# Performance work log

Hardware: AMD Instinct MI355X
Metric: run time of the kernel (lower is better)

## Reference

```python
import jax, jax.numpy as jnp
import numpy as np

T = 32400   # bs*H*W BEV queries (1*180*180)
S = 16896   # bs*num_cams*h*w image keys (1*6*32*88)
E = 256     # embed_dim
H = 8       # num_heads
D = 32      # head_dim
MAXL = 32   # max interval length (ref_num_f)


def _mlp(x, w1, b1, w2, b2):
    # nn.Sequential(Linear(E,2E), ReLU, Linear(2E,E))
    return jax.nn.relu(x @ w1 + b1) @ w2 + b2


def setup_inputs() -> dict:
    k0 = jax.random.key(0)
    ks = jax.random.split(k0, 8)
    # ragged interval structure: every BEV cell has an interval of length (idx%32)+1
    lengths = (np.arange(T) % MAXL) + 1
    starts = np.concatenate([np.zeros(1, np.int64), np.cumsum(lengths)[:-1]])
    N = int(lengths.sum())  # 534472 frustum points
    ranks_bev = np.repeat(np.arange(T), lengths)          # sorted by BEV cell
    rng = np.random.default_rng(0)
    ranks_feat = rng.integers(0, S, size=N)               # which key/value row each point reads

    def lin(k, fi, fo):
        return jax.random.normal(k, (fi, fo), jnp.float32) * (1.0 / np.sqrt(fi))

    key_feat = jax.random.normal(ks[1], (S, E), jnp.float32)
    return dict(
        query_depth=jax.random.normal(ks[0], (T, E), jnp.float32),
        key=key_feat,
        value=key_feat,  # module asserts torch.equal(key, value)
        q_w1=lin(ks[2], E, 2 * E), q_b1=jnp.zeros((2 * E,), jnp.float32),
        q_w2=lin(ks[3], 2 * E, E), q_b2=jnp.zeros((E,), jnp.float32),
        k_w1=lin(ks[4], E, 2 * E), k_b1=jnp.zeros((2 * E,), jnp.float32),
        k_w2=lin(ks[5], 2 * E, E), k_b2=jnp.zeros((E,), jnp.float32),
        ranks_feat_f=jnp.asarray(ranks_feat, jnp.int32),
        ranks_bev_f=jnp.asarray(ranks_bev, jnp.int32),
        interval_starts_f=jnp.asarray(starts, jnp.int32),
        interval_lengths_f=jnp.asarray(lengths, jnp.int32),
        ref_num=MAXL,
    )


def reference(query_depth, key, value,
              q_w1, q_b1, q_w2, q_b2,
              k_w1, k_b1, k_w2, k_b2,
              ranks_feat_f, ranks_bev_f,
              interval_starts_f, interval_lengths_f, ref_num):
    scaling = 1.0 / jnp.sqrt(jnp.float32(D))
    q = (_mlp(query_depth, q_w1, q_b1, q_w2, q_b2) * scaling).reshape(T, H, D)
    k = _mlp(key, k_w1, k_b1, k_w2, k_b2).reshape(S, H, D)
    v = value.reshape(S, H, D)

    N = ranks_bev_f.shape[0]
    pt = jnp.arange(N, dtype=jnp.int32)
    # interval id of each point (intervals are contiguous, sorted by start)
    iid = jnp.searchsorted(interval_starts_f, pt, side='right') - 1
    ranks_ref = pt - interval_starts_f[iid]  # within-interval slot, in [0, ref_num)

    # per-point raw attention logit: q[bev] . k[feat] per head  -> [N, H]
    w = jnp.einsum('nhd,nhd->nh', q[ranks_bev_f], k[ranks_feat_f])

    # scatter into ragged weight tensor [T, H, ref_num]; padding masked to -1e9
    attn = jnp.full((T, H, ref_num), -1e9, jnp.float32)
    attn = attn.at[ranks_bev_f, :, ranks_ref].set(w)
    attn = jax.nn.softmax(attn, axis=-1)

    # gather normalized weights back per point and scatter-combine values
    wp = attn[ranks_bev_f, :, ranks_ref]          # [N, H]
    vp = v[ranks_feat_f]                          # [N, H, D]
    out = jnp.zeros((T, H, D), jnp.float32).at[ranks_bev_f].add(wp[:, :, None] * vp)
    return out.reshape(T, E)
```

## Files before the change

kernel.cpp:

```cpp
#include <hip/hip_runtime.h>
#include <hip/hip_bf16.h>
#include <cstdint>
#include <cstddef>

constexpr int T_Q   = 32400;
constexpr int T_PAD = 32512;
constexpr int S_K   = 16896;
constexpr int E_DIM = 256;
constexpr int HID   = 512;

typedef __bf16 bf16x8 __attribute__((ext_vector_type(8)));
typedef float  f32x4  __attribute__((ext_vector_type(4)));
typedef unsigned short ushort8v __attribute__((ext_vector_type(8)));

__device__ __forceinline__ void async16(const __hip_bfloat16* gp, __hip_bfloat16* lp) {
    __builtin_amdgcn_global_load_lds(
        (const __attribute__((address_space(1))) void*)(gp),
        (__attribute__((address_space(3))) void*)(lp), 16, 0, 0);
}

__device__ __forceinline__ float b2f(unsigned short u) {
    return __uint_as_float(((unsigned)u) << 16);
}

constexpr int NB_K = (S_K * E_DIM / 4) / 256;
constexpr int NB_PREP = NB_K + 128;

__global__ __launch_bounds__(256) void prep(
    const float* __restrict__ val_in,
    const float* __restrict__ s0, const float* __restrict__ s1,
    const float* __restrict__ s2, const float* __restrict__ s3,
    __hip_bfloat16* __restrict__ kvB,
    __hip_bfloat16* __restrict__ d0, __hip_bfloat16* __restrict__ d1,
    __hip_bfloat16* __restrict__ d2, __hip_bfloat16* __restrict__ d3) {
    __shared__ float tb[64][65];
    const int b = blockIdx.x;
    const int tid = threadIdx.x;

    if (b < NB_K) {
        int i = (b * 256 + tid) * 4;
        float4 f = *(const float4*)(val_in + i);
        union { ushort4 u4; __hip_bfloat16 bb[4]; } cv;
        cv.bb[0] = __float2bfloat16(f.x);
        cv.bb[1] = __float2bfloat16(f.y);
        cv.bb[2] = __float2bfloat16(f.z);
        cv.bb[3] = __float2bfloat16(f.w);
        int r = i >> 8, c = i & 255;
        *(ushort4*)(kvB + (size_t)r * 512 + 256 + c) = cv.u4;
        return;
    }

    int tloc = b - NB_K;
    int m = tloc >> 5;
    int tt = tloc & 31;
    const float* S = m == 0 ? s0 : m == 1 ? s1 : m == 2 ? s2 : s3;
    __hip_bfloat16* D = m == 0 ? d0 : m == 1 ? d1 : m == 2 ? d2 : d3;
    int Kd, Nd, kt, nt;
    if ((m & 1) == 0) { Kd = 256; Nd = 512; kt = tt & 3; nt = tt >> 2; }
    else              { Kd = 512; Nd = 256; kt = tt & 7; nt = tt >> 3; }
    int tx = tid & 63, ty = tid >> 6;
#pragma unroll
    for (int p = 0; p < 16; ++p) {
        int row = ty * 16 + p;
        tb[row][tx] = S[(size_t)(kt * 64 + row) * Nd + nt * 64 + tx];
    }
    __syncthreads();
#pragma unroll
    for (int p = 0; p < 16; ++p) {
        int row = ty * 16 + p;
        D[(size_t)(nt * 64 + row) * Kd + kt * 64 + tx] = __float2bfloat16(tb[tx][row]);
    }
}


constexpr int MLP_QT = T_PAD / 64;
constexpr int MLP_KT = S_K / 64;
constexpr int MLP_NB = MLP_QT + MLP_KT;

__global__ __launch_bounds__(512, 4) void mlp_fused(
    const float* __restrict__ Aq, const float* __restrict__ Ak,
    const __hip_bfloat16* __restrict__ W1q, const __hip_bfloat16* __restrict__ W1k,
    const __hip_bfloat16* __restrict__ W2q, const __hip_bfloat16* __restrict__ W2k,
    const float* __restrict__ b1q, const float* __restrict__ b1k,
    const float* __restrict__ b2q, const float* __restrict__ b2k,
    __hip_bfloat16* __restrict__ Cq, __hip_bfloat16* __restrict__ Ck,
    float scaleq, int qtiles) {
    __shared__ __align__(16) __hip_bfloat16 Aslab[64 * 64];
    __shared__ __align__(16) __hip_bfloat16 Bs[256 * 64];
    __shared__ __align__(16) __hip_bfloat16 Hs[64 * 256];

    const int b = blockIdx.x;
    const bool isq = b < qtiles;
    const float* A  = isq ? Aq : Ak;
    const __hip_bfloat16* W1 = isq ? W1q : W1k;
    const __hip_bfloat16* W2 = isq ? W2q : W2k;
    const float* b1 = isq ? b1q : b1k;
    const float* b2 = isq ? b2q : b2k;
    __hip_bfloat16* C = isq ? Cq : Ck;
    const int ldc = isq ? E_DIM : 512;
    const float scale = isq ? scaleq : 1.0f;
    const int mrow0 = (isq ? b : b - qtiles) * 64;
    const int rowlim = isq ? T_Q : S_K;

    const int tid = threadIdx.x;
    const int w = tid >> 6, l = tid & 63;
    const int lm = l & 15, lq = l >> 4;
    const int wm = w >> 2;
    const int wn4 = w & 3;
    const int srow8 = l >> 3;
    const int u8 = l & 7;
    const int pu8 = u8 ^ srow8;
    const int scolB = (u8 ^ srow8) << 3;

    f32x4 acc2[2][4] = {};

#pragma unroll 1
    for (int nh = 0; nh < 2; ++nh) {
        f32x4 acc[2][4] = {};
#pragma unroll 1
        for (int st = 0; st < 4; ++st) {
            const int k0 = st * 64;
            {
                int r = w * 8 + srow8;
                int gr = mrow0 + r;
                float4 f0 = make_float4(0.f, 0.f, 0.f, 0.f);
                float4 f1 = make_float4(0.f, 0.f, 0.f, 0.f);
                if (gr < rowlim) {
                    const float* ap = A + (size_t)gr * 256 + k0 + u8 * 8;
                    f0 = *(const float4*)ap;
                    f1 = *(const float4*)(ap + 4);
                }
                union { bf16x8 v; __hip_bfloat16 bb[8]; } cv;
                cv.bb[0] = __float2bfloat16(f0.x); cv.bb[1] = __float2bfloat16(f0.y);
                cv.bb[2] = __float2bfloat16(f0.z); cv.bb[3] = __float2bfloat16(f0.w);
                cv.bb[4] = __float2bfloat16(f1.x); cv.bb[5] = __float2bfloat16(f1.y);
                cv.bb[6] = __float2bfloat16(f1.z); cv.bb[7] = __float2bfloat16(f1.w);
                *(bf16x8*)(Aslab + r * 64 + pu8 * 8) = cv.v;
            }
#pragma unroll
            for (int c = 0; c < 4; ++c) {
                int r = w * 32 + c * 8 + srow8;
                async16(W1 + (size_t)(nh * 256 + r) * 256 + k0 + scolB,
                        Bs + (w * 32 + c * 8) * 64);
            }
            __syncthreads();
#pragma unroll
            for (int ks = 0; ks < 2; ++ks) {
                bf16x8 af[2], bfr[4];
#pragma unroll
                for (int mi = 0; mi < 2; ++mi) {
                    int row = wm * 32 + mi * 16 + lm;
                    int pu = (ks * 4 + lq) ^ (row & 7);
                    af[mi] = *(const bf16x8*)(Aslab + row * 64 + pu * 8);
                }
#pragma unroll
                for (int ni = 0; ni < 4; ++ni) {
                    int brow = wn4 * 64 + ni * 16 + lm;
                    int pu = (ks * 4 + lq) ^ (brow & 7);
                    bfr[ni] = *(const bf16x8*)(Bs + brow * 64 + pu * 8);
                }
#pragma unroll
                for (int mi = 0; mi < 2; ++mi)
#pragma unroll
                    for (int ni = 0; ni < 4; ++ni)
                        acc[mi][ni] = __builtin_amdgcn_mfma_f32_16x16x32_bf16(
                            af[mi], bfr[ni], acc[mi][ni], 0, 0, 0);
            }
            __syncthreads();
        }

#pragma unroll
        for (int ni = 0; ni < 4; ++ni) {
            int col = wn4 * 64 + ni * 16 + lm;
            float bv = b1[nh * 256 + col];
            int un = col >> 3, el = col & 7;
#pragma unroll
            for (int mi = 0; mi < 2; ++mi) {
#pragma unroll
                for (int r = 0; r < 4; ++r) {
                    int row = wm * 32 + mi * 16 + lq * 4 + r;
                    float vv = fmaxf(acc[mi][ni][r] + bv, 0.f);
                    int pu = (un & 24) | ((un & 7) ^ (row & 7));
                    Hs[row * 256 + pu * 8 + el] = __float2bfloat16(vv);
                }
            }
        }

#pragma unroll 1
        for (int st = 0; st < 4; ++st) {
            const int k0 = st * 64;
#pragma unroll
            for (int c = 0; c < 4; ++c) {
                int r = w * 32 + c * 8 + srow8;
                async16(W2 + (size_t)r * 512 + nh * 256 + k0 + scolB,
                        Bs + (w * 32 + c * 8) * 64);
            }
            __syncthreads();
#pragma unroll
            for (int ks = 0; ks < 2; ++ks) {
                bf16x8 af[2], bfr[4];
#pragma unroll
                for (int mi = 0; mi < 2; ++mi) {
                    int row = wm * 32 + mi * 16 + lm;
                    int un = st * 8 + ks * 4 + lq;
                    int pu = (un & 24) | ((un & 7) ^ (row & 7));
                    af[mi] = *(const bf16x8*)(Hs + row * 256 + pu * 8);
                }
#pragma unroll
                for (int ni = 0; ni < 4; ++ni) {
                    int brow = wn4 * 64 + ni * 16 + lm;
                    int pu = (ks * 4 + lq) ^ (brow & 7);
                    bfr[ni] = *(const bf16x8*)(Bs + brow * 64 + pu * 8);
                }
#pragma unroll
                for (int mi = 0; mi < 2; ++mi)
#pragma unroll
                    for (int ni = 0; ni < 4; ++ni)
                        acc2[mi][ni] = __builtin_amdgcn_mfma_f32_16x16x32_bf16(
                            af[mi], bfr[ni], acc2[mi][ni], 0, 0, 0);
            }
            __syncthreads();
        }
    }

#pragma unroll
    for (int ni = 0; ni < 4; ++ni) {
        int col = wn4 * 64 + ni * 16 + lm;
        float bv = b2[col];
#pragma unroll
        for (int mi = 0; mi < 2; ++mi) {
            size_t rowb = (size_t)mrow0 + wm * 32 + mi * 16 + lq * 4;
#pragma unroll
            for (int r = 0; r < 4; ++r) {
                float vv = (acc2[mi][ni][r] + bv) * scale;
                C[(rowb + r) * ldc + col] = __float2bfloat16(vv);
            }
        }
    }
}


#define PREFP(KB, VB, C)                                                     \
    {                                                                        \
        int f_ = __shfl(myf, (C) + half);                                    \
        const __hip_bfloat16* p_ = kv + ((size_t)f_ << 9) + (sub << 3);      \
        KB = *(const ushort8v*)p_;                                           \
        VB = *(const ushort8v*)(p_ + 256);                                   \
    }

#define PROCP(KB, VB, C)                                                     \
    {                                                                        \
        float wv = 0.f;                                                      \
        _Pragma("unroll") for (int i = 0; i < 8; ++i)                        \
            wv = fmaf(qf[i], b2f(KB[i]), wv);                                \
        wv += __shfl_xor(wv, 1);                                             \
        wv += __shfl_xor(wv, 2);                                             \
        float sc = ((C) + half < L) ? wv : -1e30f;                           \
        float so = __shfl_xor(sc, 32);                                       \
        float pm = fmaxf(sc, so);                                            \
        if (__all(pm <= m)) {                                                \
            float p = __expf(sc - m);                                        \
            s += p;                                                          \
            _Pragma("unroll") for (int i = 0; i < 8; ++i)                    \
                a[i] = fmaf(p, b2f(VB[i]), a[i]);                            \
        } else {                                                             \
            float mn = fmaxf(m, pm);                                         \
            float al = __expf(m - mn);                                       \
            float p  = __expf(sc - mn);                                      \
            m = mn;                                                          \
            s = fmaf(s, al, p);                                              \
            _Pragma("unroll") for (int i = 0; i < 8; ++i)                    \
                a[i] = fmaf(p, b2f(VB[i]), a[i] * al);                       \
        }                                                                    \
    }

#define STEPP(KB, VB, J)                                                     \
    if (c + (J) < L) {                                                       \
        PROCP(KB, VB, c + (J));                                              \
        if (c + (J) + 8 < L) PREFP(KB, VB, c + (J) + 8);                     \
    }

constexpr int ATTN_BLOCKS = 2026;

__global__ __launch_bounds__(256) void attn_kernel(
    const __hip_bfloat16* __restrict__ q,
    const __hip_bfloat16* __restrict__ kv,
    const int* __restrict__ rf,
    const int* __restrict__ starts,
    const int* __restrict__ lens,
    float* __restrict__ out) {
    const int wid = threadIdx.x >> 6;
    const int l = threadIdx.x & 63;
    const int sub = l & 31, half = l >> 5;
    const int tstride = gridDim.x * 4;

    for (int t = blockIdx.x * 4 + wid; t < T_Q; t += tstride) {
        int su = __builtin_amdgcn_readfirstlane(starts[t]);
        int L  = __builtin_amdgcn_readfirstlane(lens[t]);

        int li = l < L - 1 ? l : L - 1;
        int myf = rf[su + li];

        ushort8v qu = *(const ushort8v*)(q + (size_t)t * 256 + sub * 8);
        float qf[8];
#pragma unroll
        for (int i = 0; i < 8; ++i) qf[i] = b2f(qu[i]);

        float m = -INFINITY, s = 0.f;
        float a[8] = {0.f, 0.f, 0.f, 0.f, 0.f, 0.f, 0.f, 0.f};

        ushort8v k0 = {}, v0 = {}, k1 = {}, v1 = {};
        ushort8v k2 = {}, v2 = {}, k3 = {}, v3 = {};
        PREFP(k0, v0, 0);
        if (L > 2) PREFP(k1, v1, 2);
        if (L > 4) PREFP(k2, v2, 4);
        if (L > 6) PREFP(k3, v3, 6);

        for (int c = 0; c < L; c += 8) {
            STEPP(k0, v0, 0)
            STEPP(k1, v1, 2)
            STEPP(k2, v2, 4)
            STEPP(k3, v3, 6)
        }

        float st = s + __shfl_xor(s, 32);
#pragma unroll
        for (int i = 0; i < 8; ++i) a[i] += __shfl_xor(a[i], 32);

        if (half) {
            float inv = 1.f / st;
            float* op = out + (size_t)t * 256 + sub * 8;
            float4 o0, o1;
            o0.x = a[0] * inv; o0.y = a[1] * inv; o0.z = a[2] * inv; o0.w = a[3] * inv;
            o1.x = a[4] * inv; o1.y = a[5] * inv; o1.z = a[6] * inv; o1.w = a[7] * inv;
            *(float4*)op = o0;
            *(float4*)(op + 4) = o1;
        }
    }
}

extern "C" void kernel_launch(void* const* d_in, const int* in_sizes, int n_in,
                              void* d_out, int out_size, void* d_ws, size_t ws_size,
                              hipStream_t stream) {
    const float* q_in   = (const float*)d_in[0];
    const float* key_in = (const float*)d_in[1];
    const float* val_in = (const float*)d_in[2];
    const float* q_w1   = (const float*)d_in[3];
    const float* q_b1   = (const float*)d_in[4];
    const float* q_w2   = (const float*)d_in[5];
    const float* q_b2   = (const float*)d_in[6];
    const float* k_w1   = (const float*)d_in[7];
    const float* k_b1   = (const float*)d_in[8];
    const float* k_w2   = (const float*)d_in[9];
    const float* k_b2   = (const float*)d_in[10];
    const int* ranks_feat = (const int*)d_in[11];
    const int* starts     = (const int*)d_in[13];
    const int* lens       = (const int*)d_in[14];
    float* out = (float*)d_out;

    char* ws = (char*)d_ws;
    size_t off = 0;
    auto alloc = [&](size_t bytes) {
        char* p = ws + off;
        off += (bytes + 255) & ~(size_t)255;
        return p;
    };
    __hip_bfloat16* qMl  = (__hip_bfloat16*)alloc((size_t)T_PAD * E_DIM * 2);
    __hip_bfloat16* kvB  = (__hip_bfloat16*)alloc((size_t)S_K * 512 * 2);
    __hip_bfloat16* w1qT = (__hip_bfloat16*)alloc((size_t)HID * E_DIM * 2);
    __hip_bfloat16* w2qT = (__hip_bfloat16*)alloc((size_t)E_DIM * HID * 2);
    __hip_bfloat16* w1kT = (__hip_bfloat16*)alloc((size_t)HID * E_DIM * 2);
    __hip_bfloat16* w2kT = (__hip_bfloat16*)alloc((size_t)E_DIM * HID * 2);
    (void)ws_size; (void)n_in; (void)out_size; (void)in_sizes;

    prep<<<NB_PREP, 256, 0, stream>>>(val_in, q_w1, q_w2, k_w1, k_w2,
                                      kvB, w1qT, w2qT, w1kT, w2kT);

    const float qscale = 0.17677669529663687f;

    mlp_fused<<<MLP_NB, 512, 0, stream>>>(
        q_in, key_in, w1qT, w1kT, w2qT, w2kT,
        q_b1, k_b1, q_b2, k_b2, qMl, kvB, qscale, MLP_QT);

    attn_kernel<<<ATTN_BLOCKS, 256, 0, stream>>>(qMl, kvB, ranks_feat, starts, lens, out);
}
```

Before: 273.4 us.

## Double-buffer MLP weight tiles and preload full input slab into LDS

The fused MLP kernel now stages the whole 64x256 input row slab into LDS once, converted to bf16, instead of reloading a 64-column slice at each K step. Weight tiles for W1 and W2 are ping-ponged between two LDS buffers, so the next tile's async global-to-LDS load is issued before the MFMA work on the current tile. The aim is to hide weight-load latency behind compute and remove one barrier per step. In exchange, LDS use grows to about 128KB per block and the launch-bounds occupancy hint is dropped, which likely allows fewer resident blocks per CU.

New measurement: 270.6 us. No clear change (-1.1%).

```diff
diff --git a/kernel.cpp b/kernel.cpp
--- a/kernel.cpp
+++ b/kernel.cpp
@@ -77,7 +77,7 @@
 constexpr int MLP_KT = S_K / 64;
 constexpr int MLP_NB = MLP_QT + MLP_KT;
 
-__global__ __launch_bounds__(512, 4) void mlp_fused(
+__global__ __launch_bounds__(512) void mlp_fused(
     const float* __restrict__ Aq, const float* __restrict__ Ak,
     const __hip_bfloat16* __restrict__ W1q, const __hip_bfloat16* __restrict__ W1k,
     const __hip_bfloat16* __restrict__ W2q, const __hip_bfloat16* __restrict__ W2k,
@@ -85,9 +85,9 @@
     const float* __restrict__ b2q, const float* __restrict__ b2k,
     __hip_bfloat16* __restrict__ Cq, __hip_bfloat16* __restrict__ Ck,
     float scaleq, int qtiles) {
-    __shared__ __align__(16) __hip_bfloat16 Aslab[64 * 64];
-    __shared__ __align__(16) __hip_bfloat16 Bs[256 * 64];
+    __shared__ __align__(16) __hip_bfloat16 As[64 * 256];
     __shared__ __align__(16) __hip_bfloat16 Hs[64 * 256];
+    __shared__ __align__(16) __hip_bfloat16 Bsbuf[2][256 * 64];
 
     const int b = blockIdx.x;
     const bool isq = b < qtiles;
@@ -109,9 +109,50 @@
     const int wn4 = w & 3;
     const int srow8 = l >> 3;
     const int u8 = l & 7;
-    const int pu8 = u8 ^ srow8;
     const int scolB = (u8 ^ srow8) << 3;
 
+    auto issueW1 = [&](int nh, int st, int bi) {
+#pragma unroll
+        for (int c = 0; c < 4; ++c) {
+            int r = w * 32 + c * 8 + srow8;
+            async16(W1 + (size_t)(nh * 256 + r) * 256 + st * 64 + scolB,
+                    Bsbuf[bi] + (w * 32 + c * 8) * 64);
+        }
+    };
+    auto issueW2 = [&](int nh, int st, int bi) {
+#pragma unroll
+        for (int c = 0; c < 4; ++c) {
+            int r = w * 32 + c * 8 + srow8;
+            async16(W2 + (size_t)r * 512 + nh * 256 + st * 64 + scolB,
+                    Bsbuf[bi] + (w * 32 + c * 8) * 64);
+        }
+    };
+
+    issueW1(0, 0, 0);
+#pragma unroll
+    for (int c = 0; c < 4; ++c) {
+        int idx = tid + c * 512;
+        int row = idx >> 5;
+        int u = idx & 31;
+        int gr = mrow0 + row;
+        float4 f0 = make_float4(0.f, 0.f, 0.f, 0.f);
+        float4 f1 = make_float4(0.f, 0.f, 0.f, 0.f);
+        if (gr < rowlim) {
+            const float* ap = A + (size_t)gr * 256 + u * 8;
+            f0 = *(const float4*)ap;
+            f1 = *(const float4*)(ap + 4);
+        }
+        union { bf16x8 v; __hip_bfloat16 bb[8]; } cv;
+        cv.bb[0] = __float2bfloat16(f0.x); cv.bb[1] = __float2bfloat16(f0.y);
+        cv.bb[2] = __float2bfloat16(f0.z); cv.bb[3] = __float2bfloat16(f0.w);
+        cv.bb[4] = __float2bfloat16(f1.x); cv.bb[5] = __float2bfloat16(f1.y);
+        cv.bb[6] = __float2bfloat16(f1.z); cv.bb[7] = __float2bfloat16(f1.w);
+        int pu = (u & 24) | ((u & 7) ^ (row & 7));
+        *(bf16x8*)(As + row * 256 + pu * 8) = cv.v;
+    }
+    __syncthreads();
+
+    int cur = 0;
     f32x4 acc2[2][4] = {};
 
 #pragma unroll 1
@@ -119,45 +160,24 @@
         f32x4 acc[2][4] = {};
 #pragma unroll 1
         for (int st = 0; st < 4; ++st) {
-            const int k0 = st * 64;
-            {
-                int r = w * 8 + srow8;
-                int gr = mrow0 + r;
-                float4 f0 = make_float4(0.f, 0.f, 0.f, 0.f);
-                float4 f1 = make_float4(0.f, 0.f, 0.f, 0.f);
-                if (gr < rowlim) {
-                    const float* ap = A + (size_t)gr * 256 + k0 + u8 * 8;
-                    f0 = *(const float4*)ap;
-                    f1 = *(const float4*)(ap + 4);
-                }
-                union { bf16x8 v; __hip_bfloat16 bb[8]; } cv;
-                cv.bb[0] = __float2bfloat16(f0.x); cv.bb[1] = __float2bfloat16(f0.y);
-                cv.bb[2] = __float2bfloat16(f0.z); cv.bb[3] = __float2bfloat16(f0.w);
-                cv.bb[4] = __float2bfloat16(f1.x); cv.bb[5] = __float2bfloat16(f1.y);
-                cv.bb[6] = __float2bfloat16(f1.z); cv.bb[7] = __float2bfloat16(f1.w);
-                *(bf16x8*)(Aslab + r * 64 + pu8 * 8) = cv.v;
-            }
-#pragma unroll
-            for (int c = 0; c < 4; ++c) {
-                int r = w * 32 + c * 8 + srow8;
-                async16(W1 + (size_t)(nh * 256 + r) * 256 + k0 + scolB,
-                        Bs + (w * 32 + c * 8) * 64);
-            }
-            __syncthreads();
+            if (st < 3) issueW1(nh, st + 1, cur ^ 1);
+            else        issueW2(nh, 0, cur ^ 1);
+            const __hip_bfloat16* Bb = Bsbuf[cur];
 #pragma unroll
             for (int ks = 0; ks < 2; ++ks) {
                 bf16x8 af[2], bfr[4];
 #pragma unroll
                 for (int mi = 0; mi < 2; ++mi) {
                     int row = wm * 32 + mi * 16 + lm;
-                    int pu = (ks * 4 + lq) ^ (row & 7);
-                    af[mi] = *(const bf16x8*)(Aslab + row * 64 + pu * 8);
+                    int un = st * 8 + ks * 4 + lq;
+                    int pu = (un & 24) | ((un & 7) ^ (row & 7));
+                    af[mi] = *(const bf16x8*)(As + row * 256 + pu * 8);
                 }
 #pragma unroll
                 for (int ni = 0; ni < 4; ++ni) {
                     int brow = wn4 * 64 + ni * 16 + lm;
                     int pu = (ks * 4 + lq) ^ (brow & 7);
-                    bfr[ni] = *(const bf16x8*)(Bs + brow * 64 + pu * 8);
+                    bfr[ni] = *(const bf16x8*)(Bb + brow * 64 + pu * 8);
                 }
 #pragma unroll
                 for (int mi = 0; mi < 2; ++mi)
@@ -167,6 +187,7 @@
                             af[mi], bfr[ni], acc[mi][ni], 0, 0, 0);
             }
             __syncthreads();
+            cur ^= 1;
         }
 
 #pragma unroll
@@ -185,17 +206,13 @@
                 }
             }
         }
+        __syncthreads();
 
 #pragma unroll 1
         for (int st = 0; st < 4; ++st) {
-            const int k0 = st * 64;
-#pragma unroll
-            for (int c = 0; c < 4; ++c) {
-                int r = w * 32 + c * 8 + srow8;
-                async16(W2 + (size_t)r * 512 + nh * 256 + k0 + scolB,
-                        Bs + (w * 32 + c * 8) * 64);
-            }
-            __syncthreads();
+            if (st < 3)          issueW2(nh, st + 1, cur ^ 1);
+            else if (nh == 0)    issueW1(1, 0, cur ^ 1);
+            const __hip_bfloat16* Bb = Bsbuf[cur];
 #pragma unroll
             for (int ks = 0; ks < 2; ++ks) {
                 bf16x8 af[2], bfr[4];
@@ -210,7 +227,7 @@
                 for (int ni = 0; ni < 4; ++ni) {
                     int brow = wn4 * 64 + ni * 16 + lm;
                     int pu = (ks * 4 + lq) ^ (brow & 7);
-                    bfr[ni] = *(const bf16x8*)(Bs + brow * 64 + pu * 8);
+                    bfr[ni] = *(const bf16x8*)(Bb + brow * 64 + pu * 8);
                 }
 #pragma unroll
                 for (int mi = 0; mi < 2; ++mi)
@@ -220,6 +237,7 @@
                             af[mi], bfr[ni], acc2[mi][ni], 0, 0, 0);
             }
             __syncthreads();
+            cur ^= 1;
         }
     }
 
```
